# Performance work log

Hardware: AMD Instinct MI355X
Metric: run time of the kernel (lower is better)

The kernel has to match this reference:

```python
import jax, jax.numpy as jnp
import numpy as np

KS = 3                 # kernel_size
DILATIONS = (1, 2, 3)  # dilation list
NUM_HEADS = 6


def _unfold_reflect(x, ks, dil):
    """ReflectionPad2d(dil*(ks-1)//2) + Unfold(ks, dilation=dil).
    x: [B, C, H, W] -> [B, C*ks*ks, H, W] (channel-major like torch Unfold)."""
    pad = dil * (ks - 1) // 2
    xp = jnp.pad(x, ((0, 0), (0, 0), (pad, pad), (pad, pad)), mode='reflect')
    return jax.lax.conv_general_dilated_patches(
        xp, filter_shape=(ks, ks), window_strides=(1, 1), padding='VALID',
        rhs_dilation=(dil, dil))  # [B, C*ks*ks, H, W]


def _dilate_attention(q, k, v, head_dim, ks, dil):
    """q,k,v: [B, c2, H, W] -> [B, H, W, c2]."""
    B, c2, H, W = q.shape
    nh = c2 // head_dim
    scale = head_dim ** (-0.5)
    P = H * W
    k2 = ks * ks
    # q -> [B, nh, P, hd]
    qr = q.reshape(B, nh, head_dim, P).transpose(0, 1, 3, 2)
    # unfold k, v -> [B, c2*k2, H, W], channel order (c, kh, kw)
    ku = _unfold_reflect(k, ks, dil).reshape(B, nh, head_dim, k2, P)
    vu = _unfold_reflect(v, ks, dil).reshape(B, nh, head_dim, k2, P)
    kr = ku.transpose(0, 1, 4, 2, 3)  # [B, nh, P, hd, k2]
    vr = vu.transpose(0, 1, 4, 3, 2)  # [B, nh, P, k2, hd]
    scores = jnp.einsum('bnpd,bnpdk->bnpk', qr, kr) * scale
    attn = jax.nn.softmax(scores, axis=-1)
    out = jnp.einsum('bnpk,bnpkd->bnpd', attn, vr)  # [B, nh, P, hd]
    return out.transpose(0, 2, 1, 3).reshape(B, H, W, nh * head_dim)


def _forward(x, pos_w, pos_b, qkv_w, proj_w):
    B, C, H, W = x.shape
    nd = len(DILATIONS)
    c2 = C // nd
    head_dim = C // NUM_HEADS
    # depthwise 3x3 positional conv (groups=C) + residual
    pe = jax.lax.conv_general_dilated(
        x, pos_w, window_strides=(1, 1), padding=((1, 1), (1, 1)),
        dimension_numbers=('NCHW', 'OIHW', 'NCHW'), feature_group_count=C)
    x = x + pe + pos_b[None, :, None, None]
    # 1x1 qkv conv
    qkv = jnp.einsum('oc,bchw->bohw', qkv_w, x)  # [B, 3C, H, W]
    # 'b (three nd c2) h w -> nd three b c2 h w'
    qkv = qkv.reshape(B, 3, nd, c2, H, W).transpose(2, 1, 0, 3, 4, 5)
    outs = []
    for i, dil in enumerate(DILATIONS):
        o = _dilate_attention(qkv[i, 0], qkv[i, 1], qkv[i, 2], head_dim, KS, dil)
        outs.append(o.transpose(0, 3, 1, 2))  # [B, c2, H, W]
    xo = jnp.concatenate(outs, axis=1)  # [B, C, H, W], dilation-major channels
    return jnp.einsum('oc,bchw->bohw', proj_w, xo)


def setup_inputs() -> dict:
    key = jax.random.key(0)
    ks = jax.random.split(key, 5)
    B, C, H, W = 4, 192, 128, 128
    return {
        'x': jax.random.normal(ks[0], (B, C, H, W), dtype=jnp.float32),
        'pos_w': jax.random.normal(ks[1], (C, 1, 3, 3), dtype=jnp.float32) * 0.05,
        'pos_b': jax.random.normal(ks[2], (C,), dtype=jnp.float32) * 0.05,
        'qkv_w': jax.random.normal(ks[3], (3 * C, C), dtype=jnp.float32) * (C ** -0.5),
        'proj_w': jax.random.normal(ks[4], (C, C), dtype=jnp.float32) * (C ** -0.5),
    }


def reference(x, pos_w, pos_b, qkv_w, proj_w):
    return _forward(x, pos_w, pos_b, qkv_w, proj_w)
```

## Files before the change

kernel.cpp:

```cpp
#include <hip/hip_runtime.h>
#include <hip/hip_bf16.h>
#include <math.h>

#define Hdim 128
#define Wdim 128
#define HW   16384
#define Cdim 192
#define Bdim 4
#define QKVC 576
#define NTOT (Bdim * HW)

typedef __attribute__((ext_vector_type(8))) short short8;
typedef __attribute__((ext_vector_type(4))) short short4v;
typedef __attribute__((ext_vector_type(4))) float f32x4;

__device__ __forceinline__ void async_ld16(void* lds, const void* g) {
    __builtin_amdgcn_global_load_lds(
        (const __attribute__((address_space(1))) void*)g,
        (__attribute__((address_space(3))) void*)lds, 16, 0, 0);
}
__device__ __forceinline__ float lo16(unsigned u) { return __uint_as_float(u << 16); }
__device__ __forceinline__ float hi16(unsigned u) { return __uint_as_float(u & 0xffff0000u); }

__global__ void convert_w(const float* __restrict__ qkv_w,
                          const float* __restrict__ proj_w,
                          __hip_bfloat16* __restrict__ Wq,
                          __hip_bfloat16* __restrict__ Wp) {
    int i = blockIdx.x * 256 + threadIdx.x;
    if (i < QKVC * Cdim) {
        Wq[i] = __float2bfloat16(qkv_w[i]);
    } else {
        int j = i - QKVC * Cdim;
        Wp[j] = __float2bfloat16(proj_w[j]);
    }
}

__global__ __launch_bounds__(256, 5)
void posconv_nhwc(const float* __restrict__ x,
                  const float* __restrict__ pos_w,
                  const float* __restrict__ pos_b,
                  __hip_bfloat16* __restrict__ Xb) {
    __shared__ __align__(16) float xs[3 * 16 * 128];
    __shared__ __hip_bfloat16 tile[16][132];

    int t = threadIdx.x;
    int id = blockIdx.x;
    int xj = id & 7;
    int r_ = id >> 3;
    int rb = r_ & 15;
    int cg = (r_ >> 4) % 12;
    int b  = (r_ >> 4) / 12;
    int h  = xj * 16 + rb;

    int hh0 = h > 0 ? h - 1 : 0;
    int hh1 = h;
    int hh2 = h < Hdim - 1 ? h + 1 : Hdim - 1;

    int ch = t >> 4;
    int qh = t & 15;
    int cglob = cg * 16 + ch;

    const float* wp = pos_w + cglob * 9;
    float w0 = wp[0], w1 = wp[1], w2 = wp[2];
    float w3 = wp[3], w4 = wp[4], w5 = wp[5];
    float w6 = wp[6], w7 = wp[7], w8 = wp[8];
    float bias = pos_b[cglob];
    float m0 = (h > 0) ? 1.f : 0.f;
    float m2 = (h < Hdim - 1) ? 1.f : 0.f;
    w0 *= m0; w1 *= m0; w2 *= m0;
    w6 *= m2; w7 *= m2; w8 *= m2;

    {
        const float* xg = x + (size_t)(b * Cdim + cg * 16) * HW;
#pragma unroll
        for (int k = 0; k < 6; ++k) {
            int u = t + k * 256;
            int rowi = u >> 5;
            int ql = u & 31;
            int rr = rowi >> 4;
            int sch = rowi & 15;
            int hr = rr == 0 ? hh0 : (rr == 1 ? hh1 : hh2);
            int qs = ql ^ sch;
            async_ld16((char*)xs + (size_t)u * 16,
                       xg + (size_t)sch * HW + hr * Wdim + qs * 4);
        }
    }
    __syncthreads();

    float out[8];
    {
        const char* xsb = (const char*)xs;
        const char* r0b = xsb + (size_t)(0 * 16 + ch) * 512;
        const char* r1b = xsb + (size_t)(1 * 16 + ch) * 512;
        const char* r2b = xsb + (size_t)(2 * 16 + ch) * 512;
        float4 lo0 = *(const float4*)(r0b + (((2 * qh)     ^ ch) * 16));
        float4 hi0 = *(const float4*)(r0b + (((2 * qh + 1) ^ ch) * 16));
        float4 lo1 = *(const float4*)(r1b + (((2 * qh)     ^ ch) * 16));
        float4 hi1 = *(const float4*)(r1b + (((2 * qh + 1) ^ ch) * 16));
        float4 lo2 = *(const float4*)(r2b + (((2 * qh)     ^ ch) * 16));
        float4 hi2 = *(const float4*)(r2b + (((2 * qh + 1) ^ ch) * 16));
        float L0 = __shfl_up(hi0.w, 1, 64), R0 = __shfl_down(lo0.x, 1, 64);
        float L1 = __shfl_up(hi1.w, 1, 64), R1 = __shfl_down(lo1.x, 1, 64);
        float L2 = __shfl_up(hi2.w, 1, 64), R2 = __shfl_down(lo2.x, 1, 64);
        if (qh == 0)  { L0 = 0.f; L1 = 0.f; L2 = 0.f; }
        if (qh == 15) { R0 = 0.f; R1 = 0.f; R2 = 0.f; }
        float a0[10] = {L0, lo0.x, lo0.y, lo0.z, lo0.w, hi0.x, hi0.y, hi0.z, hi0.w, R0};
        float a1[10] = {L1, lo1.x, lo1.y, lo1.z, lo1.w, hi1.x, hi1.y, hi1.z, hi1.w, R1};
        float a2[10] = {L2, lo2.x, lo2.y, lo2.z, lo2.w, hi2.x, hi2.y, hi2.z, hi2.w, R2};
#pragma unroll
        for (int i = 0; i < 8; ++i) {
            out[i] = a1[i + 1] + bias
                   + w0 * a0[i] + w1 * a0[i + 1] + w2 * a0[i + 2]
                   + w3 * a1[i] + w4 * a1[i + 1] + w5 * a1[i + 2]
                   + w6 * a2[i] + w7 * a2[i + 1] + w8 * a2[i + 2];
        }
    }

    union { unsigned short u[8]; short8 v; } pk;
#pragma unroll
    for (int i = 0; i < 8; ++i) {
        __hip_bfloat16 bv = __float2bfloat16(out[i]);
        pk.u[i] = *(unsigned short*)&bv;
    }
    *(short8*)(void*)&tile[ch][qh * 8] = pk.v;
    __syncthreads();

    int px = t >> 1, s2 = t & 1;
    union { unsigned short u[8]; short8 v; } o;
#pragma unroll
    for (int j = 0; j < 8; ++j)
        o.u[j] = *(const unsigned short*)&tile[s2 * 8 + j][px];
    size_t p0img = (size_t)(b << 14) + (size_t)h * Wdim;
    *(short8*)(void*)(Xb + (p0img + px) * Cdim + cg * 16 + s2 * 8) = o.v;
}

template <int MODE, int MT>
__global__ __launch_bounds__(256, 3)
void gemm_mfma(const __hip_bfloat16* __restrict__ Wb,
               const __hip_bfloat16* __restrict__ Xt,
               void* __restrict__ Cout) {
    __shared__ __hip_bfloat16 As[2][64 * 32];
    __shared__ __hip_bfloat16 Bs[2][256 * 32];
    const int t = threadIdx.x;
    const int w = t >> 6, l = t & 63;
    const int lq = l >> 4, lr = l & 15;
    const int id = blockIdx.x;
    const int xj = id & 7;
    const int rest = id >> 3;
    const int m0 = (rest % MT) * 64;
    const int n0 = ((rest / MT) * 8 + xj) * 256;

    const int ms = t >> 2, kcs = t & 3;

    auto stage = [&](int buf, int kt_) {
        const int k0_ = kt_ * 32;
        async_ld16(As[buf] + t * 8,
                   Wb + (size_t)(m0 + ms) * Cdim + k0_ + kcs * 8);
#pragma unroll
        for (int it = 0; it < 4; ++it) {
            int idx = it * 256 + t;
            int n = idx >> 2, kc = idx & 3;
            const __hip_bfloat16* src;
            if (MODE == 0)
                src = Xt + (size_t)(n0 + n) * Cdim + k0_ + kc * 8;
            else
                src = Xt + (size_t)kt_ * ((size_t)NTOT * 32) +
                      (size_t)(n0 + n) * 32 + kc * 8;
            async_ld16(Bs[buf] + idx * 8, src);
        }
    };

    f32x4 acc[4][4] = {};

    stage(0, 0);
    __syncthreads();

#pragma unroll
    for (int kt = 0; kt < 6; ++kt) {
        const int cur = kt & 1;
        if (kt < 5) stage(cur ^ 1, kt + 1);

        short8 af[4], bf[4];
#pragma unroll
        for (int i = 0; i < 4; ++i)
            af[i] = *(const short8*)(void*)(As[cur] + (i * 16 + lr) * 32 + lq * 8);
#pragma unroll
        for (int j = 0; j < 4; ++j)
            bf[j] = *(const short8*)(void*)(Bs[cur] + (w * 64 + j * 16 + lr) * 32 + lq * 8);
#pragma unroll
        for (int i = 0; i < 4; ++i)
#pragma unroll
            for (int j = 0; j < 4; ++j)
                acc[i][j] = __builtin_amdgcn_mfma_f32_16x16x32_bf16(
                    af[i], bf[j], acc[i][j], 0, 0, 0);

        __syncthreads();
    }

#pragma unroll
    for (int i = 0; i < 4; ++i) {
        int mb = m0 + i * 16 + lq * 4;
#pragma unroll
        for (int j = 0; j < 4; ++j) {
            int n = n0 + w * 64 + j * 16 + lr;
            if (MODE == 0) {
                int three = mb / 192, rem = mb % 192;
                int pi = rem >> 6, pn = (rem >> 5) & 1, d4 = rem & 31;
                size_t plane = (size_t)((three * 3 + pi) * 2 + pn);
                __hip_bfloat16* dst = (__hip_bfloat16*)Cout +
                    plane * ((size_t)NTOT * 32) + (size_t)n * 32 + d4;
                short4v pk;
#pragma unroll
                for (int r = 0; r < 4; ++r) {
                    __hip_bfloat16 bv = __float2bfloat16(acc[i][j][r]);
                    pk[r] = *(short*)&bv;
                }
                *(short4v*)(void*)dst = pk;
            } else {
                int b = n >> 14, p = n & (HW - 1);
#pragma unroll
                for (int r = 0; r < 4; ++r)
                    ((float*)Cout)[((size_t)(b * Cdim + mb + r)) * HW + p] =
                        acc[i][j][r];
            }
        }
    }
}

__global__ __launch_bounds__(256, 3)
void attn_kernel(const __hip_bfloat16* __restrict__ QKV,
                 __hip_bfloat16* __restrict__ AO) {
    __shared__ __align__(16) unsigned char lds[6][8192];

    int t = threadIdx.x;
    int pix = t >> 1, s = t & 1;
    int id = blockIdx.x;
    int xj = id & 7;
    int rest = id >> 3;
    int cb = rest >> 4;
    int k16 = rest & 15;
    int h = xj * 16 + k16;
    int b = cb / 6, comb = cb % 6;
    int dil = (comb >> 1) + 1;

    int w = pix;
    int col = (b << 14) + h * Wdim + w;

    const size_t PS = (size_t)NTOT * 32;
    const __hip_bfloat16* Qp = QKV + (size_t)comb * PS;
    const __hip_bfloat16* Kp = Qp + 6 * PS;
    const __hip_bfloat16* Vp = Qp + 12 * PS;

    const uint4* qp = (const uint4*)(Qp + (size_t)col * 32) + s * 2;
    uint4 qv0 = qp[0], qv1 = qp[1];

    int hh[3];
#pragma unroll
    for (int kh = 0; kh < 3; ++kh) {
        int v = h + (kh - 1) * dil;
        hh[kh] = v < 0 ? -v : (v >= Hdim ? 2 * Hdim - 2 - v : v);
    }
    int j0 = t, j1 = t + 256;
    int g0 = j0 ^ ((j0 >> 3) & 7);
    int g1 = j1 ^ ((j1 >> 3) & 7);
#pragma unroll
    for (int r = 0; r < 3; ++r) {
        size_t rowe = ((size_t)(b << 14) + (size_t)hh[r] * Wdim) * 32;
        async_ld16(&lds[r][j0 * 16],     Kp + rowe + g0 * 8);
        async_ld16(&lds[r][j1 * 16],     Kp + rowe + g1 * 8);
        async_ld16(&lds[r + 3][j0 * 16], Vp + rowe + g0 * 8);
        async_ld16(&lds[r + 3][j1 * 16], Vp + rowe + g1 * 8);
    }
    __syncthreads();

    float q[16];
    {
        uint4 x = qv0;
        q[0] = lo16(x.x); q[1] = hi16(x.x);
        q[2] = lo16(x.y); q[3] = hi16(x.y);
        q[4] = lo16(x.z); q[5] = hi16(x.z);
        q[6] = lo16(x.w); q[7] = hi16(x.w);
        x = qv1;
        q[8]  = lo16(x.x); q[9]  = hi16(x.x);
        q[10] = lo16(x.y); q[11] = hi16(x.y);
        q[12] = lo16(x.z); q[13] = hi16(x.z);
        q[14] = lo16(x.w); q[15] = hi16(x.w);
    }

    int coff[3];
#pragma unroll
    for (int kw = 0; kw < 3; ++kw) {
        int ww = w + (kw - 1) * dil;
        ww = ww < 0 ? -ww : (ww >= Wdim ? 2 * Wdim - 2 - ww : ww);
        int i0 = 4 * ww + 2 * s;
        coff[kw] = (i0 ^ ((ww >> 1) & 7)) * 16;
    }

    float sc[9];
#pragma unroll
    for (int kh = 0; kh < 3; ++kh)
#pragma unroll
        for (int kw = 0; kw < 3; ++kw) {
            uint4 xa = *(const uint4*)(void*)&lds[kh][coff[kw]];
            uint4 xb = *(const uint4*)(void*)&lds[kh][coff[kw] ^ 16];
            float p0 = 0.f;
            p0 += q[0] * lo16(xa.x) + q[1] * hi16(xa.x);
            p0 += q[2] * lo16(xa.y) + q[3] * hi16(xa.y);
            p0 += q[4] * lo16(xa.z) + q[5] * hi16(xa.z);
            p0 += q[6] * lo16(xa.w) + q[7] * hi16(xa.w);
            p0 += q[8]  * lo16(xb.x) + q[9]  * hi16(xb.x);
            p0 += q[10] * lo16(xb.y) + q[11] * hi16(xb.y);
            p0 += q[12] * lo16(xb.z) + q[13] * hi16(xb.z);
            p0 += q[14] * lo16(xb.w) + q[15] * hi16(xb.w);
            sc[kh * 3 + kw] = p0;
        }

#pragma unroll
    for (int j = 0; j < 9; ++j)
        sc[j] = (sc[j] + __shfl_xor(sc[j], 1, 64)) * 0.17677669529663687f;

    float m = sc[0];
#pragma unroll
    for (int j = 1; j < 9; ++j) m = fmaxf(m, sc[j]);
    float sum = 0.f;
#pragma unroll
    for (int j = 0; j < 9; ++j) { sc[j] = __expf(sc[j] - m); sum += sc[j]; }
    float inv = 1.f / sum;

    float acc[16] = {};
#pragma unroll
    for (int kh = 0; kh < 3; ++kh)
#pragma unroll
        for (int kw = 0; kw < 3; ++kw) {
            float a = sc[kh * 3 + kw];
            uint4 xa = *(const uint4*)(void*)&lds[kh + 3][coff[kw]];
            uint4 xb = *(const uint4*)(void*)&lds[kh + 3][coff[kw] ^ 16];
            acc[0] += a * lo16(xa.x); acc[1] += a * hi16(xa.x);
            acc[2] += a * lo16(xa.y); acc[3] += a * hi16(xa.y);
            acc[4] += a * lo16(xa.z); acc[5] += a * hi16(xa.z);
            acc[6] += a * lo16(xa.w); acc[7] += a * hi16(xa.w);
            acc[8]  += a * lo16(xb.x); acc[9]  += a * hi16(xb.x);
            acc[10] += a * lo16(xb.y); acc[11] += a * hi16(xb.y);
            acc[12] += a * lo16(xb.z); acc[13] += a * hi16(xb.z);
            acc[14] += a * lo16(xb.w); acc[15] += a * hi16(xb.w);
        }

    union { unsigned short hu[16]; short8 v[2]; } o;
#pragma unroll
    for (int d = 0; d < 16; ++d) {
        __hip_bfloat16 bv = __float2bfloat16(acc[d] * inv);
        o.hu[d] = *(unsigned short*)&bv;
    }
    short8* dst = (short8*)(void*)(AO + (size_t)comb * PS + (size_t)col * 32 + s * 16);
#pragma unroll
    for (int u = 0; u < 2; ++u) dst[u] = o.v[u];
}

extern "C" void kernel_launch(void* const* d_in, const int* in_sizes, int n_in,
                              void* d_out, int out_size, void* d_ws, size_t ws_size,
                              hipStream_t stream) {
    const float* x      = (const float*)d_in[0];
    const float* pos_w  = (const float*)d_in[1];
    const float* pos_b  = (const float*)d_in[2];
    const float* qkv_w  = (const float*)d_in[3];
    const float* proj_w = (const float*)d_in[4];
    float* out = (float*)d_out;

    char* ws = (char*)d_ws;
    __hip_bfloat16* Xb  = (__hip_bfloat16*)ws;
    __hip_bfloat16* QKV = (__hip_bfloat16*)(ws + (size_t)25165824);
    __hip_bfloat16* AO  = (__hip_bfloat16*)(ws + (size_t)100663296);
    __hip_bfloat16* Wq  = (__hip_bfloat16*)(ws + (size_t)125829120);
    __hip_bfloat16* Wp  = (__hip_bfloat16*)(ws + (size_t)126050304);

    convert_w<<<(QKVC * Cdim + Cdim * Cdim) / 256, 256, 0, stream>>>(
        qkv_w, proj_w, Wq, Wp);

    posconv_nhwc<<<6144, 256, 0, stream>>>(x, pos_w, pos_b, Xb);

    gemm_mfma<0, 9><<<2304, 256, 0, stream>>>(Wq, Xb, QKV);

    attn_kernel<<<3072, 256, 0, stream>>>(QKV, AO);

    gemm_mfma<1, 3><<<768, 256, 0, stream>>>(Wp, AO, out);
}
```

Measured before the change: 188.6 us.

## Fuse dilated attention with output projection in one row-tiled kernel

```diff
diff --git a/kernel.cpp b/kernel.cpp
--- a/kernel.cpp
+++ b/kernel.cpp
@@ -227,133 +227,156 @@
     }
 }
 
-__global__ __launch_bounds__(256, 3)
-void attn_kernel(const __hip_bfloat16* __restrict__ QKV,
-                 __hip_bfloat16* __restrict__ AO) {
-    __shared__ __align__(16) unsigned char lds[6][8192];
-
-    int t = threadIdx.x;
-    int pix = t >> 1, s = t & 1;
-    int id = blockIdx.x;
-    int xj = id & 7;
-    int rest = id >> 3;
-    int cb = rest >> 4;
-    int k16 = rest & 15;
-    int h = xj * 16 + k16;
-    int b = cb / 6, comb = cb % 6;
-    int dil = (comb >> 1) + 1;
-
-    int w = pix;
-    int col = (b << 14) + h * Wdim + w;
-
+__global__ __launch_bounds__(512, 2)
+void attn_proj(const __hip_bfloat16* __restrict__ QKV,
+               const __hip_bfloat16* __restrict__ Wpg,
+               float* __restrict__ out) {
+    __shared__ __align__(16) unsigned char smem[151552];
+    unsigned char* kv  = smem;
+    unsigned char* aob = smem + 98304;
+    unsigned char* wpl = smem;
+
+    const int t = threadIdx.x;
+    const int px = t >> 2, s = t & 3;
+    const int id = blockIdx.x;
+    const int xj = id & 7, rest = id >> 3;
+    const int b = rest >> 4, rb = rest & 15;
+    const int h = xj * 16 + rb;
     const size_t PS = (size_t)NTOT * 32;
-    const __hip_bfloat16* Qp = QKV + (size_t)comb * PS;
-    const __hip_bfloat16* Kp = Qp + 6 * PS;
-    const __hip_bfloat16* Vp = Qp + 12 * PS;
-
-    const uint4* qp = (const uint4*)(Qp + (size_t)col * 32) + s * 2;
-    uint4 qv0 = qp[0], qv1 = qp[1];
-
-    int hh[3];
-#pragma unroll
-    for (int kh = 0; kh < 3; ++kh) {
-        int v = h + (kh - 1) * dil;
-        hh[kh] = v < 0 ? -v : (v >= Hdim ? 2 * Hdim - 2 - v : v);
-    }
-    int j0 = t, j1 = t + 256;
-    int g0 = j0 ^ ((j0 >> 3) & 7);
-    int g1 = j1 ^ ((j1 >> 3) & 7);
-#pragma unroll
-    for (int r = 0; r < 3; ++r) {
-        size_t rowe = ((size_t)(b << 14) + (size_t)hh[r] * Wdim) * 32;
-        async_ld16(&lds[r][j0 * 16],     Kp + rowe + g0 * 8);
-        async_ld16(&lds[r][j1 * 16],     Kp + rowe + g1 * 8);
-        async_ld16(&lds[r + 3][j0 * 16], Vp + rowe + g0 * 8);
-        async_ld16(&lds[r + 3][j1 * 16], Vp + rowe + g1 * 8);
-    }
+    const size_t colbase = (size_t)(b << 14) + (size_t)h * Wdim;
+
+    uint4 qv[6];
+#pragma unroll
+    for (int c = 0; c < 6; ++c)
+        qv[c] = *((const uint4*)(QKV + (size_t)c * PS + (colbase + px) * 32) + s);
+
+    const int g = t ^ ((t >> 3) & 7);
+
+    auto stageKV = [&](int buf, int comb) {
+        int dil = (comb >> 1) + 1;
+        unsigned char* base = kv + buf * 49152;
+#pragma unroll
+        for (int kh = 0; kh < 3; ++kh) {
+            int v = h + (kh - 1) * dil;
+            v = v < 0 ? -v : (v >= Hdim ? 2 * Hdim - 2 - v : v);
+            size_t rowe = ((size_t)(b << 14) + (size_t)v * Wdim) * 32;
+            async_ld16(base + (kh * 512 + t) * 16,
+                       QKV + (size_t)(6 + comb) * PS + rowe + g * 8);
+            async_ld16(base + ((kh + 3) * 512 + t) * 16,
+                       QKV + (size_t)(12 + comb) * PS + rowe + g * 8);
+        }
+    };
+
+    stageKV(0, 0);
     __syncthreads();
 
-    float q[16];
-    {
-        uint4 x = qv0;
-        q[0] = lo16(x.x); q[1] = hi16(x.x);
-        q[2] = lo16(x.y); q[3] = hi16(x.y);
-        q[4] = lo16(x.z); q[5] = hi16(x.z);
-        q[6] = lo16(x.w); q[7] = hi16(x.w);
-        x = qv1;
-        q[8]  = lo16(x.x); q[9]  = hi16(x.x);
-        q[10] = lo16(x.y); q[11] = hi16(x.y);
-        q[12] = lo16(x.z); q[13] = hi16(x.z);
-        q[14] = lo16(x.w); q[15] = hi16(x.w);
-    }
-
-    int coff[3];
-#pragma unroll
-    for (int kw = 0; kw < 3; ++kw) {
-        int ww = w + (kw - 1) * dil;
-        ww = ww < 0 ? -ww : (ww >= Wdim ? 2 * Wdim - 2 - ww : ww);
-        int i0 = 4 * ww + 2 * s;
-        coff[kw] = (i0 ^ ((ww >> 1) & 7)) * 16;
-    }
-
-    float sc[9];
-#pragma unroll
-    for (int kh = 0; kh < 3; ++kh)
-#pragma unroll
-        for (int kw = 0; kw < 3; ++kw) {
-            uint4 xa = *(const uint4*)(void*)&lds[kh][coff[kw]];
-            uint4 xb = *(const uint4*)(void*)&lds[kh][coff[kw] ^ 16];
-            float p0 = 0.f;
-            p0 += q[0] * lo16(xa.x) + q[1] * hi16(xa.x);
-            p0 += q[2] * lo16(xa.y) + q[3] * hi16(xa.y);
-            p0 += q[4] * lo16(xa.z) + q[5] * hi16(xa.z);
-            p0 += q[6] * lo16(xa.w) + q[7] * hi16(xa.w);
-            p0 += q[8]  * lo16(xb.x) + q[9]  * hi16(xb.x);
-            p0 += q[10] * lo16(xb.y) + q[11] * hi16(xb.y);
-            p0 += q[12] * lo16(xb.z) + q[13] * hi16(xb.z);
-            p0 += q[14] * lo16(xb.w) + q[15] * hi16(xb.w);
-            sc[kh * 3 + kw] = p0;
-        }
-
-#pragma unroll
-    for (int j = 0; j < 9; ++j)
-        sc[j] = (sc[j] + __shfl_xor(sc[j], 1, 64)) * 0.17677669529663687f;
-
-    float m = sc[0];
-#pragma unroll
-    for (int j = 1; j < 9; ++j) m = fmaxf(m, sc[j]);
-    float sum = 0.f;
-#pragma unroll
-    for (int j = 0; j < 9; ++j) { sc[j] = __expf(sc[j] - m); sum += sc[j]; }
-    float inv = 1.f / sum;
-
-    float acc[16] = {};
-#pragma unroll
-    for (int kh = 0; kh < 3; ++kh)
-#pragma unroll
-        for (int kw = 0; kw < 3; ++kw) {
-            float a = sc[kh * 3 + kw];
-            uint4 xa = *(const uint4*)(void*)&lds[kh + 3][coff[kw]];
-            uint4 xb = *(const uint4*)(void*)&lds[kh + 3][coff[kw] ^ 16];
-            acc[0] += a * lo16(xa.x); acc[1] += a * hi16(xa.x);
-            acc[2] += a * lo16(xa.y); acc[3] += a * hi16(xa.y);
-            acc[4] += a * lo16(xa.z); acc[5] += a * hi16(xa.z);
-            acc[6] += a * lo16(xa.w); acc[7] += a * hi16(xa.w);
-            acc[8]  += a * lo16(xb.x); acc[9]  += a * hi16(xb.x);
-            acc[10] += a * lo16(xb.y); acc[11] += a * hi16(xb.y);
-            acc[12] += a * lo16(xb.z); acc[13] += a * hi16(xb.z);
-            acc[14] += a * lo16(xb.w); acc[15] += a * hi16(xb.w);
-        }
-
-    union { unsigned short hu[16]; short8 v[2]; } o;
-#pragma unroll
-    for (int d = 0; d < 16; ++d) {
-        __hip_bfloat16 bv = __float2bfloat16(acc[d] * inv);
-        o.hu[d] = *(unsigned short*)&bv;
-    }
-    short8* dst = (short8*)(void*)(AO + (size_t)comb * PS + (size_t)col * 32 + s * 16);
-#pragma unroll
-    for (int u = 0; u < 2; ++u) dst[u] = o.v[u];
+#pragma unroll
+    for (int c = 0; c < 6; ++c) {
+        if (c < 5) stageKV((c + 1) & 1, c + 1);
+
+        {
+            const int dil = (c >> 1) + 1;
+            const unsigned char* base = kv + (c & 1) * 49152;
+            float q[8];
+            {
+                uint4 x = qv[c];
+                q[0] = lo16(x.x); q[1] = hi16(x.x);
+                q[2] = lo16(x.y); q[3] = hi16(x.y);
+                q[4] = lo16(x.z); q[5] = hi16(x.z);
+                q[6] = lo16(x.w); q[7] = hi16(x.w);
+            }
+            int coff[3];
+#pragma unroll
+            for (int kw = 0; kw < 3; ++kw) {
+                int ww = px + (kw - 1) * dil;
+                ww = ww < 0 ? -ww : (ww >= Wdim ? 2 * Wdim - 2 - ww : ww);
+                int i0 = 4 * ww + s;
+                coff[kw] = (i0 ^ ((i0 >> 3) & 7)) * 16;
+            }
+            float sc[9];
+#pragma unroll
+            for (int kh = 0; kh < 3; ++kh)
+#pragma unroll
+                for (int kw = 0; kw < 3; ++kw) {
+                    uint4 xk = *(const uint4*)(void*)(base + kh * 8192 + coff[kw]);
+                    sc[kh * 3 + kw] =
+                          q[0] * lo16(xk.x) + q[1] * hi16(xk.x)
+                        + q[2] * lo16(xk.y) + q[3] * hi16(xk.y)
+                        + q[4] * lo16(xk.z) + q[5] * hi16(xk.z)
+                        + q[6] * lo16(xk.w) + q[7] * hi16(xk.w);
+                }
+#pragma unroll
+            for (int j = 0; j < 9; ++j) {
+                float v = sc[j];
+                v += __shfl_xor(v, 1, 64);
+                v += __shfl_xor(v, 2, 64);
+                sc[j] = v * 0.17677669529663687f;
+            }
+            float mx = sc[0];
+#pragma unroll
+            for (int j = 1; j < 9; ++j) mx = fmaxf(mx, sc[j]);
+            float sum = 0.f;
+#pragma unroll
+            for (int j = 0; j < 9; ++j) { sc[j] = __expf(sc[j] - mx); sum += sc[j]; }
+            float inv = 1.f / sum;
+
+            float a8[8] = {};
+#pragma unroll
+            for (int kh = 0; kh < 3; ++kh)
+#pragma unroll
+                for (int kw = 0; kw < 3; ++kw) {
+                    float a = sc[kh * 3 + kw];
+                    uint4 xv = *(const uint4*)(void*)(base + (kh + 3) * 8192 + coff[kw]);
+                    a8[0] += a * lo16(xv.x); a8[1] += a * hi16(xv.x);
+                    a8[2] += a * lo16(xv.y); a8[3] += a * hi16(xv.y);
+                    a8[4] += a * lo16(xv.z); a8[5] += a * hi16(xv.z);
+                    a8[6] += a * lo16(xv.w); a8[7] += a * hi16(xv.w);
+                }
+            union { unsigned short u[8]; short8 v; } pk;
+#pragma unroll
+            for (int d2 = 0; d2 < 8; ++d2) {
+                __hip_bfloat16 bv = __float2bfloat16(a8[d2] * inv);
+                pk.u[d2] = *(unsigned short*)&bv;
+            }
+            *(short8*)(void*)(aob + px * 416 + c * 64 + s * 16) = pk.v;
+        }
+        __syncthreads();
+    }
+
+#pragma unroll
+    for (int k = 0; k < 10; ++k) {
+        if (k < 9 || t < 384) {
+            int cidx = t + k * 512;
+            int row = cidx / 26, c16 = cidx % 26;
+            async_ld16(wpl + (size_t)cidx * 16, Wpg + row * 192 + c16 * 8);
+        }
+    }
+    __syncthreads();
+
+    const int wv = t >> 6, l = t & 63;
+    const int lq = l >> 4, lr = l & 15;
+    f32x4 pacc[12] = {};
+#pragma unroll
+    for (int kt = 0; kt < 6; ++kt) {
+        short8 bfrag = *(const short8*)(void*)
+            (aob + (wv * 16 + lr) * 416 + kt * 64 + lq * 16);
+#pragma unroll
+        for (int i = 0; i < 12; ++i) {
+            short8 afrag = *(const short8*)(void*)
+                (wpl + (i * 16 + lr) * 416 + kt * 64 + lq * 16);
+            pacc[i] = __builtin_amdgcn_mfma_f32_16x16x32_bf16(
+                afrag, bfrag, pacc[i], 0, 0, 0);
+        }
+    }
+    float* outp = out + (size_t)b * Cdim * HW + (size_t)h * Wdim;
+#pragma unroll
+    for (int i = 0; i < 12; ++i) {
+        int o = i * 16 + lq * 4;
+        int pxn = wv * 16 + lr;
+#pragma unroll
+        for (int r = 0; r < 4; ++r)
+            outp[(size_t)(o + r) * HW + pxn] = pacc[i][r];
+    }
 }
 
 extern "C" void kernel_launch(void* const* d_in, const int* in_sizes, int n_in,
@@ -369,7 +392,6 @@
     char* ws = (char*)d_ws;
     __hip_bfloat16* Xb  = (__hip_bfloat16*)ws;
     __hip_bfloat16* QKV = (__hip_bfloat16*)(ws + (size_t)25165824);
-    __hip_bfloat16* AO  = (__hip_bfloat16*)(ws + (size_t)100663296);
     __hip_bfloat16* Wq  = (__hip_bfloat16*)(ws + (size_t)125829120);
     __hip_bfloat16* Wp  = (__hip_bfloat16*)(ws + (size_t)126050304);
 
@@ -380,7 +402,5 @@
 
     gemm_mfma<0, 9><<<2304, 256, 0, stream>>>(Wq, Xb, QKV);
 
-    attn_kernel<<<3072, 256, 0, stream>>>(QKV, AO);
-
-    gemm_mfma<1, 3><<<768, 256, 0, stream>>>(Wp, AO, out);
-}
+    attn_proj<<<512, 512, 0, stream>>>(QKV, Wp, out);
+}
```

After: 178.9 us. 1.05x faster.
